# Kernel optimization log

Measured on AMD Instinct MI355X. Metric: run time of the kernel, lower is better.

Reference implementation:

```python
import jax, jax.numpy as jnp
import numpy as np
import math

BATCH, SEQLEN, DMODEL, NSTATE, DFF = 4, 2048, 1024, 16, 4096
EPS = 1e-6


def rmsnorm(x, scale):
    return x * jax.lax.rsqrt(jnp.mean(x * x, axis=-1, keepdims=True) + EPS) * scale


def ssm_scan(u, A_ssm, B_ssm, C_ssm, D_ssm):
    # u: (B, L, D). Diagonal SSM per (d, n) channel/state pair.
    dt = jnp.exp(jnp.linspace(math.log(0.001), math.log(0.1), NSTATE))  # (N,)
    expA = jnp.exp(A_ssm)                 # (D, N); continuous A = -expA
    dA = jnp.exp(-expA * dt)              # (D, N) discrete decay
    dB = B_ssm * (1.0 - dA) / expA        # (D, N) ZOH input matrix

    def step(s, u_t):
        # s: (B, D, N), u_t: (B, D)
        s = s * dA + u_t[..., None] * dB
        y = jnp.einsum('bdn,dn->bd', s, C_ssm)
        return s, y

    s0 = jnp.zeros((u.shape[0], DMODEL, NSTATE), dtype=u.dtype)
    _, ys = jax.lax.scan(step, s0, jnp.transpose(u, (1, 0, 2)))  # ys: (L, B, D)
    return jnp.transpose(ys, (1, 0, 2)) + u * D_ssm


def setup_inputs() -> dict:
    key = jax.random.key(0)
    ks = jax.random.split(key, 6)
    return {
        'x': jax.random.normal(ks[0], (BATCH, SEQLEN, DMODEL), jnp.float32),
        'A_ssm': jax.random.normal(ks[1], (DMODEL, NSTATE), jnp.float32),
        'B_ssm': jax.random.normal(ks[2], (DMODEL, NSTATE), jnp.float32),
        'C_ssm': jax.random.normal(ks[3], (DMODEL, NSTATE), jnp.float32),
        'D_ssm': jnp.zeros((DMODEL,), jnp.float32),
        'scale1': jnp.ones((DMODEL,), jnp.float32),
        'scale2': jnp.ones((DMODEL,), jnp.float32),
        'w1': jax.random.normal(ks[4], (DMODEL, DFF), jnp.float32) * 0.02,
        'b1': jnp.zeros((DFF,), jnp.float32),
        'w2': jax.random.normal(ks[5], (DFF, DMODEL), jnp.float32) * 0.02,
        'b2': jnp.zeros((DMODEL,), jnp.float32),
    }


def reference(x, A_ssm, B_ssm, C_ssm, D_ssm, scale1, scale2, w1, b1, w2, b2):
    x = x + ssm_scan(rmsnorm(x, scale1), A_ssm, B_ssm, C_ssm, D_ssm)
    h = rmsnorm(x, scale2)
    h = jax.nn.gelu(h @ w1 + b1, approximate=False) @ w2 + b2
    return x + h
```

## Files before the change

### kernel.cpp

```cpp
#include <hip/hip_runtime.h>
#include <cstdint>
#include <cstddef>


#define BATCH 4
#define SEQLEN 2048
#define DMODEL 1024
#define NSTATE 16
#define DFF 4096
#define NCH 32
#define LCH 64

typedef unsigned short ushort_t;
typedef __attribute__((ext_vector_type(8))) short short8;
typedef __attribute__((ext_vector_type(4))) float f32x4;

__device__ __forceinline__ ushort_t f2bf(float f) {
  uint32_t u = __builtin_bit_cast(uint32_t, f);
  uint32_t r = (u + 0x7FFFu + ((u >> 16) & 1u)) >> 16;
  return (ushort_t)r;
}

__global__ void coef_kernel(const float* __restrict__ A_ssm, const float* __restrict__ B_ssm,
                            const float* __restrict__ C_ssm,
                            float* __restrict__ dA_t, float* __restrict__ dBz_t,
                            float* __restrict__ dAc_t, float* __restrict__ Ct) {
  int d = blockIdx.x * 256 + threadIdx.x;
  if (d >= DMODEL) return;
  const float l0 = -6.907755278982137f;
  const float ld = 0.30701134573253947f;
  for (int n = 0; n < NSTATE; n++) {
    float dt = expf(l0 + (float)n * ld);
    float a  = A_ssm[d * NSTATE + n];
    float ea = expf(a);
    float da = expf(-ea * dt);
    float dbz = B_ssm[d * NSTATE + n] * (1.f - da) / ea;
    float dac = expf(-ea * dt * (float)LCH);
    dA_t [n * DMODEL + d] = da;
    dBz_t[n * DMODEL + d] = dbz;
    dAc_t[n * DMODEL + d] = dac;
    Ct   [n * DMODEL + d] = C_ssm[d * NSTATE + n];
  }
}

__global__ void transpose_to_bf16(const float* __restrict__ src, ushort_t* __restrict__ dst,
                                  int R, int C) {
  __shared__ float tile[32][33];
  int bx = blockIdx.x * 32, by = blockIdx.y * 32;
  int tx = threadIdx.x, ty = threadIdx.y;
  #pragma unroll
  for (int i = 0; i < 4; i++) {
    int r = by + ty + i * 8;
    tile[ty + i * 8][tx] = src[(size_t)r * C + bx + tx];
  }
  __syncthreads();
  #pragma unroll
  for (int i = 0; i < 4; i++) {
    int c = bx + ty + i * 8;
    dst[(size_t)c * R + by + tx] = f2bf(tile[tx][ty + i * 8]);
  }
}

__global__ void rms1_kernel(const float* __restrict__ x, float* __restrict__ rrms) {
  int row = blockIdx.x * 4 + (threadIdx.x >> 6);
  int lane = threadIdx.x & 63;
  const float4* p = (const float4*)(x + (size_t)row * DMODEL);
  float s = 0.f;
  #pragma unroll
  for (int w = 0; w < 4; w++) {
    float4 v = p[w * 64 + lane];
    s += v.x * v.x + v.y * v.y + v.z * v.z + v.w * v.w;
  }
  #pragma unroll
  for (int off = 32; off; off >>= 1) s += __shfl_xor(s, off, 64);
  if (lane == 0) rrms[row] = rsqrtf(s * (1.f / DMODEL) + 1e-6f);
}

__global__ void scan_pass1(const float* __restrict__ x, const float* __restrict__ rrms,
                           const float* __restrict__ scale1,
                           const float* __restrict__ dA_t, const float* __restrict__ dBz_t,
                           float* __restrict__ s_fin) {
  int d = blockIdx.x * 256 + threadIdx.x;
  int b = blockIdx.y, c = blockIdx.z;
  float dA[NSTATE], dBz[NSTATE], s[NSTATE];
  #pragma unroll
  for (int n = 0; n < NSTATE; n++) {
    dA[n] = dA_t[n * DMODEL + d];
    dBz[n] = dBz_t[n * DMODEL + d];
    s[n] = 0.f;
  }
  float sc1 = scale1[d];
  const float* xp = x + ((size_t)b * SEQLEN + (size_t)c * LCH) * DMODEL + d;
  const float* rp = rrms + b * SEQLEN + c * LCH;
  for (int t = 0; t < LCH; t++) {
    float u = xp[(size_t)t * DMODEL] * rp[t] * sc1;
    #pragma unroll
    for (int n = 0; n < NSTATE; n++) s[n] = fmaf(s[n], dA[n], u * dBz[n]);
  }
  #pragma unroll
  for (int n = 0; n < NSTATE; n++)
    s_fin[(((size_t)n * BATCH + b) * NCH + c) * DMODEL + d] = s[n];
}

__global__ void scan_pass2(const float* __restrict__ s_fin, const float* __restrict__ dAc_t,
                           float* __restrict__ s_in) {
  int idx = blockIdx.x * 256 + threadIdx.x;
  int d = idx & (DMODEL - 1);
  int b = (idx >> 10) & (BATCH - 1);
  int n = idx >> 12;
  float dc = dAc_t[n * DMODEL + d];
  float s = 0.f;
  for (int c = 0; c < NCH; c++) {
    size_t o = (((size_t)n * BATCH + b) * NCH + c) * DMODEL + d;
    s_in[o] = s;
    s = s_fin[o] + dc * s;
  }
}

__global__ void scan_pass3(const float* __restrict__ x, const float* __restrict__ rrms,
                           const float* __restrict__ scale1,
                           const float* __restrict__ dA_t, const float* __restrict__ dBz_t,
                           const float* __restrict__ Ct, const float* __restrict__ Dv,
                           const float* __restrict__ s_in, float* __restrict__ out) {
  int d = blockIdx.x * 256 + threadIdx.x;
  int b = blockIdx.y, c = blockIdx.z;
  float dA[NSTATE], dBz[NSTATE], Cc[NSTATE], s[NSTATE];
  #pragma unroll
  for (int n = 0; n < NSTATE; n++) {
    dA[n] = dA_t[n * DMODEL + d];
    dBz[n] = dBz_t[n * DMODEL + d];
    Cc[n] = Ct[n * DMODEL + d];
    s[n] = s_in[(((size_t)n * BATCH + b) * NCH + c) * DMODEL + d];
  }
  float sc1 = scale1[d], Dd = Dv[d];
  const float* xp = x + ((size_t)b * SEQLEN + (size_t)c * LCH) * DMODEL + d;
  const float* rp = rrms + b * SEQLEN + c * LCH;
  float* op = out + ((size_t)b * SEQLEN + (size_t)c * LCH) * DMODEL + d;
  for (int t = 0; t < LCH; t++) {
    float xv = xp[(size_t)t * DMODEL];
    float u = xv * rp[t] * sc1;
    float y = 0.f;
    #pragma unroll
    for (int n = 0; n < NSTATE; n++) {
      s[n] = fmaf(s[n], dA[n], u * dBz[n]);
      y = fmaf(Cc[n], s[n], y);
    }
    op[(size_t)t * DMODEL] = xv + y + u * Dd;
  }
}

__global__ void rms2_kernel(const float* __restrict__ x2, const float* __restrict__ scale2,
                            ushort_t* __restrict__ hb) {
  int row = blockIdx.x * 4 + (threadIdx.x >> 6);
  int lane = threadIdx.x & 63;
  const float4* p = (const float4*)(x2 + (size_t)row * DMODEL);
  float4 v[4];
  float s = 0.f;
  #pragma unroll
  for (int w = 0; w < 4; w++) {
    v[w] = p[w * 64 + lane];
    s += v[w].x * v[w].x + v[w].y * v[w].y + v[w].z * v[w].z + v[w].w * v[w].w;
  }
  #pragma unroll
  for (int off = 32; off; off >>= 1) s += __shfl_xor(s, off, 64);
  float r = rsqrtf(s * (1.f / DMODEL) + 1e-6f);
  const float4* sc = (const float4*)scale2;
  #pragma unroll
  for (int w = 0; w < 4; w++) {
    float4 scv = sc[w * 64 + lane];
    ushort4 u;
    u.x = f2bf(v[w].x * r * scv.x);
    u.y = f2bf(v[w].y * r * scv.y);
    u.z = f2bf(v[w].z * r * scv.z);
    u.w = f2bf(v[w].w * r * scv.w);
    *(ushort4*)(hb + (size_t)row * DMODEL + (size_t)(w * 64 + lane) * 4) = u;
  }
}


#define BKG 32

template <int N>
__device__ __forceinline__ void fence_vm() {
  asm volatile("s_waitcnt vmcnt(%0)" :: "n"(N) : "memory");
}

__device__ __forceinline__ void gl2lds16(const ushort_t* g, ushort_t* l) {
  __builtin_amdgcn_global_load_lds(
      (const __attribute__((address_space(1))) unsigned int*)g,
      (__attribute__((address_space(3))) unsigned int*)l, 16, 0, 0);
}

template <int BM, int BN, int WM, int WN, int MODE>
__global__ __launch_bounds__(512, 2) void gemm_cv(const ushort_t* __restrict__ A,
                                                  const ushort_t* __restrict__ B,
                                                  const float* __restrict__ bias,
                                                  const float* __restrict__ resid,
                                                  void* __restrict__ outp,
                                                  int M, int N, int K) {
  constexpr int NSLOT = 4;
  constexpr int TILEA = BM * BKG;
  constexpr int TILEB = BN * BKG;
  constexpr int SLOT  = TILEA + TILEB;
  constexpr int NA = BM / 128;
  constexpr int NB = BN / 128;
  constexpr int LPT = NA + NB;
  constexpr int MR = BM / (WM * 16);
  constexpr int NR = BN / (WN * 16);
  __shared__ ushort_t lds[NSLOT * SLOT];

  const int tid = threadIdx.x;
  const int wave = tid >> 6, lane = tid & 63;
  const int wr = wave / WN, wc = wave % WN;

  const int nwg = gridDim.x;
  const int cpx = nwg >> 3;
  const int bid = blockIdx.x;
  const int wg  = (bid & 7) * cpx + (bid >> 3);
  const int nbn = N / BN;
  const int m0 = (wg / nbn) * BM;
  const int n0 = (wg % nbn) * BN;

  const int NT = K / BKG;

  const ushort_t* aB = A + (size_t)(m0 + (tid >> 2)) * K + (tid & 3) * 8;
  const ushort_t* bB = B + (size_t)(n0 + (tid >> 2)) * K + (tid & 3) * 8;
  const int waveOff = wave * 512;

  auto stage = [&](int slot, int t) {
    ushort_t* sA = lds + slot * SLOT;
    ushort_t* sB = sA + TILEA;
    #pragma unroll
    for (int j = 0; j < NA; j++)
      gl2lds16(aB + (size_t)t * BKG + (size_t)j * 128 * K, sA + j * 4096 + waveOff);
    #pragma unroll
    for (int j = 0; j < NB; j++)
      gl2lds16(bB + (size_t)t * BKG + (size_t)j * 128 * K, sB + j * 4096 + waveOff);
  };

  f32x4 acc[MR][NR] = {};

  stage(0, 0); stage(1, 1); stage(2, 2);

  const int r = lane & 15, c8 = (lane >> 4) * 8;

  for (int t = 0; t < NT; ++t) {
    if (t + 2 < NT)      fence_vm<2 * LPT>();
    else if (t + 1 < NT) fence_vm<LPT>();
    else                 fence_vm<0>();
    __builtin_amdgcn_s_barrier();
    if (t + 3 < NT) stage((t + 3) & 3, t + 3);

    const ushort_t* sA = lds + (t & 3) * SLOT;
    const ushort_t* sB = sA + TILEA;
    short8 bfr[NR];
    #pragma unroll
    for (int n = 0; n < NR; n++)
      bfr[n] = *(const short8*)(sB + (size_t)(wc * (BN / WN) + n * 16 + r) * BKG + c8);
    #pragma unroll
    for (int mh = 0; mh < MR; mh += 4) {
      short8 af[4];
      #pragma unroll
      for (int m = 0; m < 4; m++)
        af[m] = *(const short8*)(sA + (size_t)(wr * (BM / WM) + (mh + m) * 16 + r) * BKG + c8);
      __builtin_amdgcn_s_setprio(1);
      #pragma unroll
      for (int m = 0; m < 4; m++)
        #pragma unroll
        for (int n = 0; n < NR; n++)
          acc[mh + m][n] =
              __builtin_amdgcn_mfma_f32_16x16x32_bf16(af[m], bfr[n], acc[mh + m][n], 0, 0, 0);
      __builtin_amdgcn_s_setprio(0);
    }
  }

  const int colb = n0 + wc * (BN / WN) + r;
  const int rowb = m0 + wr * (BM / WM) + ((lane >> 4) << 2);
  #pragma unroll
  for (int n = 0; n < NR; n++) {
    int col = colb + n * 16;
    float bs = bias[col];
    #pragma unroll
    for (int m = 0; m < MR; m++) {
      int row = rowb + m * 16;
      #pragma unroll
      for (int j = 0; j < 4; j++) {
        float v = acc[m][n][j] + bs;
        size_t o = (size_t)(row + j) * N + col;
        if (MODE == 1) {
          float g = 0.5f * v * (1.f + erff(v * 0.70710678118654752f));
          ((ushort_t*)outp)[o] = f2bf(g);
        } else {
          ((float*)outp)[o] = resid[o] + v;
        }
      }
    }
  }
}

extern "C" void kernel_launch(void* const* d_in, const int* in_sizes, int n_in,
                              void* d_out, int out_size, void* d_ws, size_t ws_size,
                              hipStream_t stream) {
  (void)in_sizes; (void)n_in; (void)out_size; (void)ws_size;
  const float* x      = (const float*)d_in[0];
  const float* A_ssm  = (const float*)d_in[1];
  const float* B_ssm  = (const float*)d_in[2];
  const float* C_ssm  = (const float*)d_in[3];
  const float* D_ssm  = (const float*)d_in[4];
  const float* scale1 = (const float*)d_in[5];
  const float* scale2 = (const float*)d_in[6];
  const float* w1     = (const float*)d_in[7];
  const float* b1     = (const float*)d_in[8];
  const float* w2     = (const float*)d_in[9];
  const float* b2     = (const float*)d_in[10];
  float* out = (float*)d_out;

  char* ws = (char*)d_ws;
  float*    rrms  = (float*)(ws + 0);
  float*    dA_t  = (float*)(ws + 32768);
  float*    dBz_t = (float*)(ws + 98304);
  float*    dAc_t = (float*)(ws + 163840);
  float*    Ct    = (float*)(ws + 229376);
  float*    s_fin = (float*)(ws + 294912);
  float*    s_in  = (float*)(ws + 8683520);
  ushort_t* hb    = (ushort_t*)(ws + 17072128);
  ushort_t* w1t   = (ushort_t*)(ws + 33849344);
  ushort_t* w2t   = (ushort_t*)(ws + 42237952);
  ushort_t* gb    = (ushort_t*)(ws + 50626560);

  const int ROWS = BATCH * SEQLEN;

  coef_kernel<<<DMODEL / 256, 256, 0, stream>>>(A_ssm, B_ssm, C_ssm, dA_t, dBz_t, dAc_t, Ct);
  transpose_to_bf16<<<dim3(DFF / 32, DMODEL / 32), dim3(32, 8), 0, stream>>>(w1, w1t, DMODEL, DFF);
  transpose_to_bf16<<<dim3(DMODEL / 32, DFF / 32), dim3(32, 8), 0, stream>>>(w2, w2t, DFF, DMODEL);
  rms1_kernel<<<ROWS / 4, 256, 0, stream>>>(x, rrms);
  scan_pass1<<<dim3(DMODEL / 256, BATCH, NCH), 256, 0, stream>>>(x, rrms, scale1, dA_t, dBz_t, s_fin);
  scan_pass2<<<(BATCH * DMODEL * NSTATE) / 256, 256, 0, stream>>>(s_fin, dAc_t, s_in);
  scan_pass3<<<dim3(DMODEL / 256, BATCH, NCH), 256, 0, stream>>>(x, rrms, scale1, dA_t, dBz_t, Ct,
                                                                 D_ssm, s_in, out);
  rms2_kernel<<<ROWS / 4, 256, 0, stream>>>(out, scale2, hb);

  gemm_cv<256, 256, 2, 4, 1><<<(ROWS / 256) * (DFF / 256), 512, 0, stream>>>(
      hb, w1t, b1, nullptr, gb, ROWS, DFF, DMODEL);
  gemm_cv<256, 128, 4, 2, 2><<<(ROWS / 256) * (DMODEL / 128), 512, 0, stream>>>(
      gb, w2t, b2, out, out, ROWS, DMODEL, DFF);
}
```

Baseline: 248.4 us.

## Split GEMM K-step into two barrier-separated phases with swizzled LDS and compile-time K

Restructures the GEMM main loop so each K tile runs in two halves: the A-stage global-to-LDS copy is issued after the first fragment loads and the B-stage copy after the second, with barriers between MFMA phases so waves move in lockstep. It adds an XOR swizzle on the LDS column offset for both the global-load destination pattern and the fragment reads, to reduce bank conflicts. K becomes a template parameter so the trip count is constant and the loop can be unrolled. More barriers per iteration may cost some overlap, and the swizzle must match exactly between producer and consumer.

```diff
diff --git a/kernel.cpp b/kernel.cpp
--- a/kernel.cpp
+++ b/kernel.cpp
@@ -185,19 +185,21 @@
   asm volatile("s_waitcnt vmcnt(%0)" :: "n"(N) : "memory");
 }
 
+__device__ __forceinline__ void bar() { asm volatile("s_barrier" ::: "memory"); }
+
 __device__ __forceinline__ void gl2lds16(const ushort_t* g, ushort_t* l) {
   __builtin_amdgcn_global_load_lds(
       (const __attribute__((address_space(1))) unsigned int*)g,
       (__attribute__((address_space(3))) unsigned int*)l, 16, 0, 0);
 }
 
-template <int BM, int BN, int WM, int WN, int MODE>
+template <int BM, int BN, int WM, int WN, int MODE, int K>
 __global__ __launch_bounds__(512, 2) void gemm_cv(const ushort_t* __restrict__ A,
                                                   const ushort_t* __restrict__ B,
                                                   const float* __restrict__ bias,
                                                   const float* __restrict__ resid,
                                                   void* __restrict__ outp,
-                                                  int M, int N, int K) {
+                                                  int M, int N) {
   constexpr int NSLOT = 4;
   constexpr int TILEA = BM * BKG;
   constexpr int TILEB = BN * BKG;
@@ -207,7 +209,9 @@
   constexpr int LPT = NA + NB;
   constexpr int MR = BM / (WM * 16);
   constexpr int NR = BN / (WN * 16);
-  __shared__ ushort_t lds[NSLOT * SLOT];
+  constexpr int MH = MR / 2;
+  constexpr int NT = K / BKG;
+  __shared__ __align__(16) ushort_t lds[NSLOT * SLOT];
 
   const int tid = threadIdx.x;
   const int wave = tid >> 6, lane = tid & 63;
@@ -221,18 +225,19 @@
   const int m0 = (wg / nbn) * BM;
   const int n0 = (wg % nbn) * BN;
 
-  const int NT = K / BKG;
-
-  const ushort_t* aB = A + (size_t)(m0 + (tid >> 2)) * K + (tid & 3) * 8;
-  const ushort_t* bB = B + (size_t)(n0 + (tid >> 2)) * K + (tid & 3) * 8;
+  const int scol = 8 * ((tid & 3) ^ ((tid >> 3) & 3));
+  const ushort_t* aB = A + (size_t)(m0 + (tid >> 2)) * K + scol;
+  const ushort_t* bB = B + (size_t)(n0 + (tid >> 2)) * K + scol;
   const int waveOff = wave * 512;
 
-  auto stage = [&](int slot, int t) {
+  auto stageA = [&](int slot, int t) {
     ushort_t* sA = lds + slot * SLOT;
-    ushort_t* sB = sA + TILEA;
     #pragma unroll
     for (int j = 0; j < NA; j++)
       gl2lds16(aB + (size_t)t * BKG + (size_t)j * 128 * K, sA + j * 4096 + waveOff);
+  };
+  auto stageB = [&](int slot, int t) {
+    ushort_t* sB = lds + slot * SLOT + TILEA;
     #pragma unroll
     for (int j = 0; j < NB; j++)
       gl2lds16(bB + (size_t)t * BKG + (size_t)j * 128 * K, sB + j * 4096 + waveOff);
@@ -240,38 +245,56 @@
 
   f32x4 acc[MR][NR] = {};
 
-  stage(0, 0); stage(1, 1); stage(2, 2);
-
-  const int r = lane & 15, c8 = (lane >> 4) * 8;
-
+  stageA(0, 0); stageB(0, 0);
+  stageA(1, 1); stageB(1, 1);
+  stageA(2, 2); stageB(2, 2);
+  fence_vm<2 * LPT>();
+  bar();
+
+  const int r = lane & 15;
+  const int cswz = ((lane >> 4) * 8) ^ (((r >> 1) & 3) << 3);
+
+  #pragma unroll 4
   for (int t = 0; t < NT; ++t) {
-    if (t + 2 < NT)      fence_vm<2 * LPT>();
-    else if (t + 1 < NT) fence_vm<LPT>();
-    else                 fence_vm<0>();
-    __builtin_amdgcn_s_barrier();
-    if (t + 3 < NT) stage((t + 3) & 3, t + 3);
-
     const ushort_t* sA = lds + (t & 3) * SLOT;
     const ushort_t* sB = sA + TILEA;
-    short8 bfr[NR];
+
+    short8 bfr[NR], af[MH];
     #pragma unroll
     for (int n = 0; n < NR; n++)
-      bfr[n] = *(const short8*)(sB + (size_t)(wc * (BN / WN) + n * 16 + r) * BKG + c8);
-    #pragma unroll
-    for (int mh = 0; mh < MR; mh += 4) {
-      short8 af[4];
+      bfr[n] = *(const short8*)(sB + (size_t)(wc * (BN / WN) + n * 16 + r) * BKG + cswz);
+    #pragma unroll
+    for (int m = 0; m < MH; m++)
+      af[m] = *(const short8*)(sA + (size_t)(wr * (BM / WM) + m * 16 + r) * BKG + cswz);
+    if (t + 3 < NT) stageA((t + 3) & 3, t + 3);
+    bar();
+    __builtin_amdgcn_s_setprio(1);
+    #pragma unroll
+    for (int m = 0; m < MH; m++)
       #pragma unroll
-      for (int m = 0; m < 4; m++)
-        af[m] = *(const short8*)(sA + (size_t)(wr * (BM / WM) + (mh + m) * 16 + r) * BKG + c8);
-      __builtin_amdgcn_s_setprio(1);
+      for (int n = 0; n < NR; n++)
+        acc[m][n] = __builtin_amdgcn_mfma_f32_16x16x32_bf16(af[m], bfr[n], acc[m][n], 0, 0, 0);
+    __builtin_amdgcn_s_setprio(0);
+    bar();
+
+    short8 af2[MR - MH];
+    #pragma unroll
+    for (int m = 0; m < MR - MH; m++)
+      af2[m] = *(const short8*)(sA + (size_t)(wr * (BM / WM) + (MH + m) * 16 + r) * BKG + cswz);
+    if (t + 3 < NT) stageB((t + 3) & 3, t + 3);
+    if (t + 3 < NT)      fence_vm<2 * LPT>();
+    else if (t + 2 < NT) fence_vm<LPT>();
+    else if (t + 1 < NT) fence_vm<0>();
+    bar();
+    __builtin_amdgcn_s_setprio(1);
+    #pragma unroll
+    for (int m = 0; m < MR - MH; m++)
       #pragma unroll
-      for (int m = 0; m < 4; m++)
-        #pragma unroll
-        for (int n = 0; n < NR; n++)
-          acc[mh + m][n] =
-              __builtin_amdgcn_mfma_f32_16x16x32_bf16(af[m], bfr[n], acc[mh + m][n], 0, 0, 0);
-      __builtin_amdgcn_s_setprio(0);
-    }
+      for (int n = 0; n < NR; n++)
+        acc[MH + m][n] =
+            __builtin_amdgcn_mfma_f32_16x16x32_bf16(af2[m], bfr[n], acc[MH + m][n], 0, 0, 0);
+    __builtin_amdgcn_s_setprio(0);
+    bar();
   }
 
   const int colb = n0 + wc * (BN / WN) + r;
@@ -340,8 +363,8 @@
                                                                  D_ssm, s_in, out);
   rms2_kernel<<<ROWS / 4, 256, 0, stream>>>(out, scale2, hb);
 
-  gemm_cv<256, 256, 2, 4, 1><<<(ROWS / 256) * (DFF / 256), 512, 0, stream>>>(
-      hb, w1t, b1, nullptr, gb, ROWS, DFF, DMODEL);
-  gemm_cv<256, 128, 4, 2, 2><<<(ROWS / 256) * (DMODEL / 128), 512, 0, stream>>>(
-      gb, w2t, b2, out, out, ROWS, DMODEL, DFF);
-}
+  gemm_cv<256, 256, 2, 4, 1, DMODEL><<<(ROWS / 256) * (DFF / 256), 512, 0, stream>>>(
+      hb, w1t, b1, nullptr, gb, ROWS, DFF);
+  gemm_cv<256, 128, 4, 2, 2, DFF><<<(ROWS / 256) * (DMODEL / 128), 512, 0, stream>>>(
+      gb, w2t, b2, out, out, ROWS, DMODEL);
+}
```

Result: faster. 240.7 us (-3.1%).
